# Optimization experiments

Measured on AMD Instinct MI355X. Metric: run time of the kernel, lower is better.

The kernel has to match this reference:

```python
import jax, jax.numpy as jnp
import numpy as np

B, N, F, H, L = 256, 512, 64, 128, 2  # batch, max_nodes, feat_dim, hidden_dim, n_layers


def setup_inputs() -> dict:
    key = jax.random.key(0)
    ks = jax.random.split(key, 14)
    sc = 0.05  # small init scale, mimics nn.Linear default magnitude
    rn = lambda k, shape: jax.random.normal(k, shape, dtype=jnp.float32) * sc
    return {
        "tree_features": jax.random.normal(ks[0], (B, N, F), dtype=jnp.float32),
        "emb_W": rn(ks[1], (F, H)),
        "emb_b": rn(ks[2], (H,)),
        # stacked per-layer gate weights, [L, H, H] (input-major: y = x @ W + b)
        "Wi": rn(ks[3], (L, H, H)),
        "Wo": rn(ks[4], (L, H, H)),
        "Wc": rn(ks[5], (L, H, H)),
        "bWi": rn(ks[6], (L, H)),
        "bUi": rn(ks[7], (L, H)),
        "bWo": rn(ks[8], (L, H)),
        "bUo": rn(ks[9], (L, H)),
        "bWc": rn(ks[10], (L, H)),
        "bUc": rn(ks[11], (L, H)),
    }


def reference(tree_features, emb_W, emb_b, Wi, Wo, Wc, bWi, bUi, bWo, bUo, bWc, bUc):
    # node embedding: [B, N, F] @ [F, H] -> [B, N, H]
    h = jnp.einsum("bnf,fh->bnh", tree_features, emb_W) + emb_b
    n_layers = Wi.shape[0]
    for l in range(n_layers):
        # tree_structure=None path: each node has no children, so h_sum = 0 and
        # U_*(h_sum) contributes only its bias bU*. Forget gate is never used.
        i = jax.nn.sigmoid(jnp.einsum("bnh,hk->bnk", h, Wi[l]) + bWi[l] + bUi[l])
        o = jax.nn.sigmoid(jnp.einsum("bnh,hk->bnk", h, Wo[l]) + bWo[l] + bUo[l])
        c_tilde = jnp.tanh(jnp.einsum("bnh,hk->bnk", h, Wc[l]) + bWc[l] + bUc[l])
        c = i * c_tilde
        h = o * jnp.tanh(c)
    # mean over nodes -> [B, H]
    return jnp.mean(h, axis=1)
```

## Files before the change

### kernel.cpp

```cpp
#include <hip/hip_runtime.h>


typedef short bf16x8 __attribute__((ext_vector_type(8)));
typedef float f32x4  __attribute__((ext_vector_type(4)));

#define MFMA16(a, b, c) __builtin_amdgcn_mfma_f32_16x16x32_bf16((a), (b), (c), 0, 0, 0)

#define NEG_L2E (-1.44269504088896f)
#define TWO_L2E (2.88539008177793f)

__device__ __forceinline__ unsigned short f2bf(float f) {
    return (unsigned short)((__float_as_uint(f) + 0x8000u) >> 16);
}
__device__ __forceinline__ float frcp(float x)  { return __builtin_amdgcn_rcpf(x); }
__device__ __forceinline__ float fexp2(float x) { return __builtin_amdgcn_exp2f(x); }

__device__ __forceinline__ float act_h(float iv, float ov, float cv) {
    float ei = fexp2(iv);
    float eo = fexp2(ov);
    float u  = fexp2(cv);
    float p  = u - 1.0f;
    float q  = (1.0f + ei) * (u + 1.0f);
    float p2 = p * p, q2 = q * q;
    float t15 = 15.0f * q2;
    return (p * (t15 + p2)) * frcp((q * (6.0f * p2 + t15)) * (1.0f + eo));
}

__device__ __forceinline__ bf16x8 pack8(float4 v0, float4 v1) {
    bf16x8 a;
    a[0] = (short)f2bf(v0.x); a[1] = (short)f2bf(v0.y);
    a[2] = (short)f2bf(v0.z); a[3] = (short)f2bf(v0.w);
    a[4] = (short)f2bf(v1.x); a[5] = (short)f2bf(v1.y);
    a[6] = (short)f2bf(v1.z); a[7] = (short)f2bf(v1.w);
    return a;
}

__device__ __forceinline__ void gload_lds16(const void* gsrc, void* ldst) {
    __builtin_amdgcn_global_load_lds(
        (const __attribute__((address_space(1))) unsigned int*)gsrc,
        (__attribute__((address_space(3))) unsigned int*)ldst, 16, 0, 0);
}

__global__ void prep_frags(const float* __restrict__ embW,
                           const float* __restrict__ Wi,
                           const float* __restrict__ Wo,
                           const float* __restrict__ Wc,
                           const float* __restrict__ bWi, const float* __restrict__ bUi,
                           const float* __restrict__ bWo, const float* __restrict__ bUo,
                           const float* __restrict__ bWc, const float* __restrict__ bUc,
                           char* __restrict__ ws) {
    const int tid = threadIdx.x;
    const int fb  = blockIdx.x * 4 + (tid >> 6);
    const int l   = tid & 63;

    if (fb < 208) {
        int g  = l >> 4, c0 = l & 15;
        const float* src;
        int t, kk;
        size_t dst;
        float scale;
        if (fb < 16) {
            t = fb >> 1; kk = fb & 1;
            src = embW;
            dst = (size_t)fb * 1024;
            scale = 1.0f;
        } else {
            int r = fb - 16;
            int layer = r / 96;
            int r2 = r % 96;
            t = r2 / 12;
            int r3 = r2 % 12;
            int gate = r3 >> 2;
            kk = r3 & 3;
            const float* Ws[3] = {Wi, Wo, Wc};
            src = Ws[gate] + (size_t)layer * 128 * 128;
            dst = 16384 + (size_t)r * 1024;
            scale = (gate == 2) ? TWO_L2E : NEG_L2E;
        }
        bf16x8 v;
#pragma unroll
        for (int e = 0; e < 8; ++e) {
            int k   = kk * 32 + g * 8 + e;
            int col = t * 16 + c0;
            v[e] = (short)f2bf(scale * src[(size_t)k * 128 + col]);
        }
        *reinterpret_cast<bf16x8*>(ws + dst + (size_t)l * 16) = v;
    } else if (blockIdx.x == 52) {
        float* bias = reinterpret_cast<float*>(ws + 212992);
#pragma unroll
        for (int j = 0; j < 3; ++j) {
            int v = j * 256 + tid;
            int layer = v / 384;
            int r = v % 384;
            int gate = r >> 7;
            int c = r & 127;
            int idx = layer * 128 + c;
            float x;
            if (gate == 0)      x = NEG_L2E * (bWi[idx] + bUi[idx]);
            else if (gate == 1) x = NEG_L2E * (bWo[idx] + bUo[idx]);
            else                x = TWO_L2E * (bWc[idx] + bUc[idx]);
            bias[v] = x;
        }
    }
}

template<int S>
__device__ __forceinline__ void t_step(
        char* __restrict__ sbuf,
        const char* __restrict__ frags,
        bf16x8 (&A0)[4], bf16x8 (&A1)[4],
        unsigned short* __restrict__ slab,
        const float* __restrict__ biasf,
        float (* __restrict__ redbuf)[128],
        int w, int l, int g, int c0) {

    constexpr int L = S >> 3;
    constexpr int T = S & 7;
    const int c = T * 16 + c0;
    const float Bi = biasf[L * 384 + c];
    const float Bo = biasf[L * 384 + 128 + c];
    const float Bc = biasf[L * 384 + 256 + c];

    const bf16x8 (&A)[4] = (L == 0) ? A0 : A1;
    const char* sr = sbuf + (size_t)l * 16;

    f32x4 ai = {Bi, Bi, Bi, Bi};
    f32x4 ao = {Bo, Bo, Bo, Bo};
    f32x4 ac = {Bc, Bc, Bc, Bc};
#pragma unroll
    for (int kk = 0; kk < 4; ++kk)
        ac = MFMA16(A[kk], *reinterpret_cast<const bf16x8*>(sr + (size_t)(8 + kk) * 1024), ac);
#pragma unroll
    for (int kk = 0; kk < 4; ++kk)
        ai = MFMA16(A[kk], *reinterpret_cast<const bf16x8*>(sr + (size_t)(0 + kk) * 1024), ai);
#pragma unroll
    for (int kk = 0; kk < 4; ++kk)
        ao = MFMA16(A[kk], *reinterpret_cast<const bf16x8*>(sr + (size_t)(4 + kk) * 1024), ao);

    __syncthreads();

    if (S < 15) {
        const char* gs = frags + 16384 + (size_t)(S + 1) * 12288;
#pragma unroll
        for (int i = 0; i < 3; ++i)
            gload_lds16(gs + (size_t)(i * 4096 + w * 1024) + (size_t)l * 16,
                        sbuf + i * 4096 + w * 1024);
    }

    float hsum = 0.0f;
#pragma unroll
    for (int r = 0; r < 4; ++r) {
        float h = act_h(ai[r], ao[r], ac[r]);
        if constexpr (L == 1) {
            hsum += h;
        } else {
            slab[(g * 4 + r) * 40 + (T & 1) * 16 + c0] = f2bf(h);
        }
    }
    if constexpr (L == 0) {
        if constexpr ((T & 1) == 1)
            A1[T >> 1] = *reinterpret_cast<const bf16x8*>(&slab[c0 * 40 + g * 8]);
    } else {
        hsum += __shfl_xor(hsum, 16);
        hsum += __shfl_xor(hsum, 32);
        if (g == 0) redbuf[w][c] = hsum;
    }

    if (S < 15) __syncthreads();
}

__global__ __launch_bounds__(256, 8) void tree_enc(
        const float* __restrict__ X,
        const float* __restrict__ emb_b,
        const char*  __restrict__ frags,
        float* __restrict__ out) {

    __shared__ __align__(16) char sbuf[12288];
    __shared__ __align__(16) unsigned short slabs[4][16 * 40];
    __shared__ float redbuf[4][128];

    const int tid = threadIdx.x;
    const int w   = tid >> 6;
    const int l   = tid & 63;
    const int g   = l >> 4;
    const int c0  = l & 15;
    const int rowbase = blockIdx.x * 64 + w * 16;
    const int batch   = blockIdx.x >> 3;

    unsigned short* __restrict__ slab = slabs[w];
    const float* biasf = reinterpret_cast<const float*>(frags + 212992);

    {
        const char* gs = frags + 16384;
#pragma unroll
        for (int i = 0; i < 3; ++i)
            gload_lds16(gs + (size_t)(i * 4096 + w * 1024) + (size_t)l * 16,
                        sbuf + i * 4096 + w * 1024);
    }

    bf16x8 A0[4], A1[4];
    {
        bf16x8 afr0, afr1;
        {
            const float* xr = X + (size_t)(rowbase + c0) * 64;
            float4 v0 = *reinterpret_cast<const float4*>(xr + g * 8);
            float4 v1 = *reinterpret_cast<const float4*>(xr + g * 8 + 4);
            float4 v2 = *reinterpret_cast<const float4*>(xr + 32 + g * 8);
            float4 v3 = *reinterpret_cast<const float4*>(xr + 32 + g * 8 + 4);
            afr0 = pack8(v0, v1);
            afr1 = pack8(v2, v3);
        }
#pragma unroll
        for (int t = 0; t < 8; ++t) {
            const char* eb = frags + (size_t)(t * 2) * 1024 + (size_t)l * 16;
            bf16x8 e0 = *reinterpret_cast<const bf16x8*>(eb);
            bf16x8 e1 = *reinterpret_cast<const bf16x8*>(eb + 1024);
            const float be = emb_b[t * 16 + c0];
            f32x4 acc = {be, be, be, be};
            acc = MFMA16(afr0, e0, acc);
            acc = MFMA16(afr1, e1, acc);
#pragma unroll
            for (int r = 0; r < 4; ++r)
                slab[(g * 4 + r) * 40 + (t & 1) * 16 + c0] = f2bf(acc[r]);
            if (t & 1)
                A0[t >> 1] = *reinterpret_cast<const bf16x8*>(&slab[c0 * 40 + g * 8]);
        }
    }
    __syncthreads();

    t_step< 0>(sbuf, frags, A0, A1, slab, biasf, redbuf, w, l, g, c0);
    t_step< 1>(sbuf, frags, A0, A1, slab, biasf, redbuf, w, l, g, c0);
    t_step< 2>(sbuf, frags, A0, A1, slab, biasf, redbuf, w, l, g, c0);
    t_step< 3>(sbuf, frags, A0, A1, slab, biasf, redbuf, w, l, g, c0);
    t_step< 4>(sbuf, frags, A0, A1, slab, biasf, redbuf, w, l, g, c0);
    t_step< 5>(sbuf, frags, A0, A1, slab, biasf, redbuf, w, l, g, c0);
    t_step< 6>(sbuf, frags, A0, A1, slab, biasf, redbuf, w, l, g, c0);
    t_step< 7>(sbuf, frags, A0, A1, slab, biasf, redbuf, w, l, g, c0);
    t_step< 8>(sbuf, frags, A0, A1, slab, biasf, redbuf, w, l, g, c0);
    t_step< 9>(sbuf, frags, A0, A1, slab, biasf, redbuf, w, l, g, c0);
    t_step<10>(sbuf, frags, A0, A1, slab, biasf, redbuf, w, l, g, c0);
    t_step<11>(sbuf, frags, A0, A1, slab, biasf, redbuf, w, l, g, c0);
    t_step<12>(sbuf, frags, A0, A1, slab, biasf, redbuf, w, l, g, c0);
    t_step<13>(sbuf, frags, A0, A1, slab, biasf, redbuf, w, l, g, c0);
    t_step<14>(sbuf, frags, A0, A1, slab, biasf, redbuf, w, l, g, c0);
    t_step<15>(sbuf, frags, A0, A1, slab, biasf, redbuf, w, l, g, c0);

    __syncthreads();
    if (tid < 128) {
        float s = redbuf[0][tid] + redbuf[1][tid] + redbuf[2][tid] + redbuf[3][tid];
        atomicAdd(&out[batch * 128 + tid], s * (1.0f / 512.0f));
    }
}

extern "C" void kernel_launch(void* const* d_in, const int* in_sizes, int n_in,
                              void* d_out, int out_size, void* d_ws, size_t ws_size,
                              hipStream_t stream) {
    const float* X    = (const float*)d_in[0];
    const float* embW = (const float*)d_in[1];
    const float* embb = (const float*)d_in[2];
    const float* Wi   = (const float*)d_in[3];
    const float* Wo   = (const float*)d_in[4];
    const float* Wc   = (const float*)d_in[5];
    const float* bWi  = (const float*)d_in[6];
    const float* bUi  = (const float*)d_in[7];
    const float* bWo  = (const float*)d_in[8];
    const float* bUo  = (const float*)d_in[9];
    const float* bWc  = (const float*)d_in[10];
    const float* bUc  = (const float*)d_in[11];
    float* out = (float*)d_out;
    char*  ws  = (char*)d_ws;

    hipMemsetAsync(d_out, 0, (size_t)out_size * sizeof(float), stream);
    prep_frags<<<53, 256, 0, stream>>>(embW, Wi, Wo, Wc,
                                       bWi, bUi, bWo, bUo, bWc, bUc, ws);
    tree_enc<<<2048, 256, 0, stream>>>(X, embb, (const char*)ws, out);
}
```

Measured before the change: 58.82 us.

## Double-buffer weight fragments in LDS and defer layer-1 mean reduction

Weight fragments now live in two LDS buffers. The prefetch for step S+1 is issued at the start of step S into the other buffer, so it overlaps the MFMAs and activations of the current step. This cuts the two barriers per step down to one. The second-layer per-column sums are kept in registers and reduced with shuffles once at the end, instead of shuffling after every step. In exchange, LDS use rises by 12 KB per block, which may lower occupancy from the requested 8 blocks per CU, and register pressure grows by 8 floats.

```diff
diff --git a/kernel.cpp b/kernel.cpp
--- a/kernel.cpp
+++ b/kernel.cpp
@@ -106,23 +106,34 @@
 
 template<int S>
 __device__ __forceinline__ void t_step(
-        char* __restrict__ sbuf,
+        char* __restrict__ sb0, char* __restrict__ sb1,
         const char* __restrict__ frags,
         bf16x8 (&A0)[4], bf16x8 (&A1)[4],
         unsigned short* __restrict__ slab,
         const float* __restrict__ biasf,
-        float (* __restrict__ redbuf)[128],
+        float (&msum)[8],
         int w, int l, int g, int c0) {
 
     constexpr int L = S >> 3;
     constexpr int T = S & 7;
+    char* cur = (S & 1) ? sb1 : sb0;
+    char* nxt = (S & 1) ? sb0 : sb1;
+
+    if constexpr (S < 15) {
+        const char* gs = frags + 16384 + (size_t)(S + 1) * 12288;
+#pragma unroll
+        for (int i = 0; i < 3; ++i)
+            gload_lds16(gs + (size_t)(i * 4096 + w * 1024) + (size_t)l * 16,
+                        nxt + i * 4096 + w * 1024);
+    }
+
     const int c = T * 16 + c0;
     const float Bi = biasf[L * 384 + c];
     const float Bo = biasf[L * 384 + 128 + c];
     const float Bc = biasf[L * 384 + 256 + c];
 
     const bf16x8 (&A)[4] = (L == 0) ? A0 : A1;
-    const char* sr = sbuf + (size_t)l * 16;
+    const char* sr = cur + (size_t)l * 16;
 
     f32x4 ai = {Bi, Bi, Bi, Bi};
     f32x4 ao = {Bo, Bo, Bo, Bo};
@@ -137,36 +148,19 @@
     for (int kk = 0; kk < 4; ++kk)
         ao = MFMA16(A[kk], *reinterpret_cast<const bf16x8*>(sr + (size_t)(4 + kk) * 1024), ao);
 
-    __syncthreads();
-
-    if (S < 15) {
-        const char* gs = frags + 16384 + (size_t)(S + 1) * 12288;
-#pragma unroll
-        for (int i = 0; i < 3; ++i)
-            gload_lds16(gs + (size_t)(i * 4096 + w * 1024) + (size_t)l * 16,
-                        sbuf + i * 4096 + w * 1024);
-    }
-
-    float hsum = 0.0f;
 #pragma unroll
     for (int r = 0; r < 4; ++r) {
         float h = act_h(ai[r], ao[r], ac[r]);
         if constexpr (L == 1) {
-            hsum += h;
+            msum[T] += h;
         } else {
             slab[(g * 4 + r) * 40 + (T & 1) * 16 + c0] = f2bf(h);
         }
     }
-    if constexpr (L == 0) {
-        if constexpr ((T & 1) == 1)
-            A1[T >> 1] = *reinterpret_cast<const bf16x8*>(&slab[c0 * 40 + g * 8]);
-    } else {
-        hsum += __shfl_xor(hsum, 16);
-        hsum += __shfl_xor(hsum, 32);
-        if (g == 0) redbuf[w][c] = hsum;
-    }
-
-    if (S < 15) __syncthreads();
+    if constexpr (L == 0 && (T & 1) == 1)
+        A1[T >> 1] = *reinterpret_cast<const bf16x8*>(&slab[c0 * 40 + g * 8]);
+
+    __syncthreads();
 }
 
 __global__ __launch_bounds__(256, 8) void tree_enc(
@@ -175,7 +169,8 @@
         const char*  __restrict__ frags,
         float* __restrict__ out) {
 
-    __shared__ __align__(16) char sbuf[12288];
+    __shared__ __align__(16) char sbuf0[12288];
+    __shared__ __align__(16) char sbuf1[12288];
     __shared__ __align__(16) unsigned short slabs[4][16 * 40];
     __shared__ float redbuf[4][128];
 
@@ -195,7 +190,7 @@
 #pragma unroll
         for (int i = 0; i < 3; ++i)
             gload_lds16(gs + (size_t)(i * 4096 + w * 1024) + (size_t)l * 16,
-                        sbuf + i * 4096 + w * 1024);
+                        sbuf0 + i * 4096 + w * 1024);
     }
 
     bf16x8 A0[4], A1[4];
@@ -228,23 +223,34 @@
     }
     __syncthreads();
 
-    t_step< 0>(sbuf, frags, A0, A1, slab, biasf, redbuf, w, l, g, c0);
-    t_step< 1>(sbuf, frags, A0, A1, slab, biasf, redbuf, w, l, g, c0);
-    t_step< 2>(sbuf, frags, A0, A1, slab, biasf, redbuf, w, l, g, c0);
-    t_step< 3>(sbuf, frags, A0, A1, slab, biasf, redbuf, w, l, g, c0);
-    t_step< 4>(sbuf, frags, A0, A1, slab, biasf, redbuf, w, l, g, c0);
-    t_step< 5>(sbuf, frags, A0, A1, slab, biasf, redbuf, w, l, g, c0);
-    t_step< 6>(sbuf, frags, A0, A1, slab, biasf, redbuf, w, l, g, c0);
-    t_step< 7>(sbuf, frags, A0, A1, slab, biasf, redbuf, w, l, g, c0);
-    t_step< 8>(sbuf, frags, A0, A1, slab, biasf, redbuf, w, l, g, c0);
-    t_step< 9>(sbuf, frags, A0, A1, slab, biasf, redbuf, w, l, g, c0);
-    t_step<10>(sbuf, frags, A0, A1, slab, biasf, redbuf, w, l, g, c0);
-    t_step<11>(sbuf, frags, A0, A1, slab, biasf, redbuf, w, l, g, c0);
-    t_step<12>(sbuf, frags, A0, A1, slab, biasf, redbuf, w, l, g, c0);
-    t_step<13>(sbuf, frags, A0, A1, slab, biasf, redbuf, w, l, g, c0);
-    t_step<14>(sbuf, frags, A0, A1, slab, biasf, redbuf, w, l, g, c0);
-    t_step<15>(sbuf, frags, A0, A1, slab, biasf, redbuf, w, l, g, c0);
-
+    float msum[8];
+#pragma unroll
+    for (int t = 0; t < 8; ++t) msum[t] = 0.f;
+
+    t_step< 0>(sbuf0, sbuf1, frags, A0, A1, slab, biasf, msum, w, l, g, c0);
+    t_step< 1>(sbuf0, sbuf1, frags, A0, A1, slab, biasf, msum, w, l, g, c0);
+    t_step< 2>(sbuf0, sbuf1, frags, A0, A1, slab, biasf, msum, w, l, g, c0);
+    t_step< 3>(sbuf0, sbuf1, frags, A0, A1, slab, biasf, msum, w, l, g, c0);
+    t_step< 4>(sbuf0, sbuf1, frags, A0, A1, slab, biasf, msum, w, l, g, c0);
+    t_step< 5>(sbuf0, sbuf1, frags, A0, A1, slab, biasf, msum, w, l, g, c0);
+    t_step< 6>(sbuf0, sbuf1, frags, A0, A1, slab, biasf, msum, w, l, g, c0);
+    t_step< 7>(sbuf0, sbuf1, frags, A0, A1, slab, biasf, msum, w, l, g, c0);
+    t_step< 8>(sbuf0, sbuf1, frags, A0, A1, slab, biasf, msum, w, l, g, c0);
+    t_step< 9>(sbuf0, sbuf1, frags, A0, A1, slab, biasf, msum, w, l, g, c0);
+    t_step<10>(sbuf0, sbuf1, frags, A0, A1, slab, biasf, msum, w, l, g, c0);
+    t_step<11>(sbuf0, sbuf1, frags, A0, A1, slab, biasf, msum, w, l, g, c0);
+    t_step<12>(sbuf0, sbuf1, frags, A0, A1, slab, biasf, msum, w, l, g, c0);
+    t_step<13>(sbuf0, sbuf1, frags, A0, A1, slab, biasf, msum, w, l, g, c0);
+    t_step<14>(sbuf0, sbuf1, frags, A0, A1, slab, biasf, msum, w, l, g, c0);
+    t_step<15>(sbuf0, sbuf1, frags, A0, A1, slab, biasf, msum, w, l, g, c0);
+
+#pragma unroll
+    for (int t = 0; t < 8; ++t) {
+        float v = msum[t];
+        v += __shfl_xor(v, 16);
+        v += __shfl_xor(v, 32);
+        if (g == 0) redbuf[w][t * 16 + c0] = v;
+    }
     __syncthreads();
     if (tid < 128) {
         float s = redbuf[0][tid] + redbuf[1][tid] + redbuf[2][tid] + redbuf[3][tid];
```

After: 71.86 us. 22.2% more time.
